# Kernel tuning notes

Hardware: AMD Instinct MI355X
Metric: run time of the kernel (lower is better)

Reference implementation:

```python
import jax, jax.numpy as jnp
import numpy as np

N_NODES = 50000
N_EDGES = 600000
D_IN = 128
D_HID = 128
D_OUT = 40
EPS = 1e-5


def setup_inputs() -> dict:
    key = jax.random.key(0)
    ks = jax.random.split(key, 16)
    inp = {
        "x": jax.random.normal(ks[0], (N_NODES, D_IN), dtype=jnp.float32),
        "edge_index": jax.random.randint(ks[1], (2, N_EDGES), 0, N_NODES, dtype=jnp.int64),
    }
    dims = [(D_IN, D_HID), (D_HID, D_HID), (D_HID, D_OUT)]
    for i, (di, do) in enumerate(dims):
        s = 1.0 / np.sqrt(di)
        inp[f"W_l{i}"] = jax.random.uniform(ks[2 + 3 * i], (di, do), jnp.float32, -s, s)
        inp[f"b_l{i}"] = jax.random.uniform(ks[3 + 3 * i], (do,), jnp.float32, -s, s)
        inp[f"W_r{i}"] = jax.random.uniform(ks[4 + 3 * i], (di, do), jnp.float32, -s, s)
    for i in range(2):  # num_convs - 1 Trans (LayerNorm) blocks
        inp[f"g{i}"] = jnp.ones((D_HID,), jnp.float32)
        inp[f"be{i}"] = jnp.zeros((D_HID,), jnp.float32)
    return inp


def _sage_conv(x, src, dst, W_l, b_l, W_r):
    # mean-aggregate neighbor features at dst, then lin_l(agg) + lin_r(x)
    msg = jax.ops.segment_sum(x[src], dst, num_segments=N_NODES)  # [N, d]
    deg = jax.ops.segment_sum(jnp.ones((src.shape[0],), x.dtype), dst, num_segments=N_NODES)
    agg = msg / jnp.clip(deg, 1.0)[:, None]
    return agg @ W_l + b_l + x @ W_r


def _trans(x, g, b):
    # LayerNorm -> GELU (exact); Dropout p=0 is identity
    mu = jnp.mean(x, axis=-1, keepdims=True)
    var = jnp.mean(jnp.square(x - mu), axis=-1, keepdims=True)
    xn = (x - mu) * jax.lax.rsqrt(var + EPS) * g + b
    return jax.nn.gelu(xn, approximate=False)


def reference(x, edge_index, W_l0, b_l0, W_r0, W_l1, b_l1, W_r1, W_l2, b_l2, W_r2, g0, be0, g1, be1):
    src, dst = edge_index[0], edge_index[1]
    h = _sage_conv(x, src, dst, W_l0, b_l0, W_r0)
    h = _sage_conv(_trans(h, g0, be0), src, dst, W_l1, b_l1, W_r1)
    h = _sage_conv(_trans(h, g1, be1), src, dst, W_l2, b_l2, W_r2)
    return jax.nn.log_softmax(h, axis=1)
```

## Files before the change

### kernel.cpp

```cpp
#include <hip/hip_runtime.h>
#include <math.h>

#define N_NODES 50000
#define N_EDGES 600000
#define DF 128
#define KK 256
#define DOUT 40
#define EPSN 1e-5f
#define NB1 196

typedef __attribute__((ext_vector_type(8))) short sh8;
typedef __attribute__((ext_vector_type(4))) float f32x4;

__device__ __forceinline__ unsigned short f2b(float f) {
  unsigned u = __builtin_bit_cast(unsigned, f);
  unsigned r = u + 0x7FFFu + ((u >> 16) & 1u);
  return (unsigned short)(r >> 16);
}
__device__ __forceinline__ float b2f(unsigned short b) {
  unsigned u = ((unsigned)b) << 16;
  return __builtin_bit_cast(float, u);
}
__device__ __forceinline__ float gelu_f(float x) {
  return 0.5f * x * (1.0f + erff(x * 0.70710678118654752f));
}

__global__ __launch_bounds__(256) void k_prep(
    const int* __restrict__ ei, int* __restrict__ counts,
    const float* __restrict__ x, unsigned* __restrict__ A,
    const float* __restrict__ Wl0, const float* __restrict__ Wr0,
    const float* __restrict__ Wl1, const float* __restrict__ Wr1,
    const float* __restrict__ Wl2, const float* __restrict__ Wr2,
    unsigned short* __restrict__ WT0, unsigned short* __restrict__ WT1,
    unsigned short* __restrict__ WT2b) {
  const int b = blockIdx.x, t = threadIdx.x;
  if (b < 2344) {
    int e = b * 256 + t;
    if (e < N_EDGES) atomicAdd(&counts[ei[N_EDGES + e]], 1);
  } else if (b < 14844) {
    int i = (b - 2344) * 256 + t;
    int n = i >> 6, p = i & 63;
    float2 v = ((const float2*)x)[i];
    A[(size_t)n * 128 + 64 + p] = (unsigned)f2b(v.x) | ((unsigned)f2b(v.y) << 16);
  } else {
    int i = (b - 14844) * 256 + t;
    if (i >= 75776) return;
    if (i < 65536) {
      const float* Wl; const float* Wr; unsigned short* WT; int j;
      if (i < 32768) { j = i;         Wl = Wl0; Wr = Wr0; WT = WT0; }
      else           { j = i - 32768; Wl = Wl1; Wr = Wr1; WT = WT1; }
      int n = j >> 8, k = j & 255;
      float v = (k < DF) ? Wl[k * DF + n] : Wr[(k - DF) * DF + n];
      WT[(k >> 3) * 1024 + n * 8 + (k & 7)] = f2b(v);
    } else {
      int j = i - 65536;
      int n = j >> 7, k = j & 127;
      float v = (n < DOUT) ? Wl2[k * DOUT + n] : Wr2[k * DOUT + (n - DOUT)];
      WT2b[(k >> 3) * 640 + n * 8 + (k & 7)] = f2b(v);
    }
  }
}

__global__ __launch_bounds__(256) void k_rowptr(
    const int* __restrict__ counts,
    int* __restrict__ rowptr, int* __restrict__ cursor,
    float* __restrict__ invdeg) {
  const int t = threadIdx.x;
  const int lane = t & 63, w = t >> 6;
  __shared__ int wtot[4], wpre[4];

  int pre = 0;
  const int limit = blockIdx.x * 256;
  for (int i = t; i < limit; i += 256) pre += counts[i];
  #pragma unroll
  for (int m = 1; m < 64; m <<= 1) pre += __shfl_xor(pre, m);
  if (lane == 0) wpre[w] = pre;

  const int i = blockIdx.x * 256 + t;
  int c = (i < N_NODES) ? counts[i] : 0;
  int s = c;
  #pragma unroll
  for (int off = 1; off < 64; off <<= 1) {
    int u = __shfl_up(s, off);
    if (lane >= off) s += u;
  }
  if (lane == 63) wtot[w] = s;
  __syncthreads();
  int add = wpre[0] + wpre[1] + wpre[2] + wpre[3];
  for (int k = 0; k < w; ++k) add += wtot[k];
  if (i < N_NODES) {
    int excl = s - c + add;
    rowptr[i] = excl;
    cursor[i] = excl;
    invdeg[i] = 1.0f / (float)((c > 1) ? c : 1);
  }
  if (blockIdx.x == 0 && t == 0) rowptr[N_NODES] = N_EDGES;
}

__global__ __launch_bounds__(256) void k_fill(
    const int* __restrict__ ei, int* __restrict__ cursor, int* __restrict__ csr) {
  int e = blockIdx.x * 256 + threadIdx.x;
  if (e < N_EDGES) {
    int d = ei[N_EDGES + e];
    int p = atomicAdd(&cursor[d], 1);
    csr[p] = ei[e];
  }
}

__global__ __launch_bounds__(256) void k_agg(
    unsigned* __restrict__ A, const int* __restrict__ rowptr,
    const int* __restrict__ csr, const float* __restrict__ invdeg) {
  const int wid = (blockIdx.x * 256 + threadIdx.x) >> 6;
  const int lane = threadIdx.x & 63;
  const int sg = lane >> 4, l = lane & 15;
  const int node = wid * 4 + sg;
  const int beg = rowptr[node], end = rowptr[node + 1];
  const uint4* H4 = (const uint4*)A;

  float f0=0,f1=0,f2=0,f3=0,f4=0,f5=0,f6=0,f7=0;
  float g0=0,g1=0,g2=0,g3=0,g4=0,g5=0,g6=0,g7=0;
  int j = beg;
  for (; j + 2 <= end; j += 2) {
    int c0 = csr[j], c1 = csr[j + 1];
    uint4 p = H4[(size_t)c0 * 32 + 16 + l];
    uint4 q = H4[(size_t)c1 * 32 + 16 + l];
    f0 += b2f((unsigned short)p.x); f1 += b2f((unsigned short)(p.x >> 16));
    f2 += b2f((unsigned short)p.y); f3 += b2f((unsigned short)(p.y >> 16));
    f4 += b2f((unsigned short)p.z); f5 += b2f((unsigned short)(p.z >> 16));
    f6 += b2f((unsigned short)p.w); f7 += b2f((unsigned short)(p.w >> 16));
    g0 += b2f((unsigned short)q.x); g1 += b2f((unsigned short)(q.x >> 16));
    g2 += b2f((unsigned short)q.y); g3 += b2f((unsigned short)(q.y >> 16));
    g4 += b2f((unsigned short)q.z); g5 += b2f((unsigned short)(q.z >> 16));
    g6 += b2f((unsigned short)q.w); g7 += b2f((unsigned short)(q.w >> 16));
  }
  if (j < end) {
    uint4 p = H4[(size_t)csr[j] * 32 + 16 + l];
    f0 += b2f((unsigned short)p.x); f1 += b2f((unsigned short)(p.x >> 16));
    f2 += b2f((unsigned short)p.y); f3 += b2f((unsigned short)(p.y >> 16));
    f4 += b2f((unsigned short)p.z); f5 += b2f((unsigned short)(p.z >> 16));
    f6 += b2f((unsigned short)p.w); f7 += b2f((unsigned short)(p.w >> 16));
  }
  f0+=g0; f1+=g1; f2+=g2; f3+=g3; f4+=g4; f5+=g5; f6+=g6; f7+=g7;
  const float rd = invdeg[node];
  uint4 o;
  o.x = (unsigned)f2b(f0 * rd) | ((unsigned)f2b(f1 * rd) << 16);
  o.y = (unsigned)f2b(f2 * rd) | ((unsigned)f2b(f3 * rd) << 16);
  o.z = (unsigned)f2b(f4 * rd) | ((unsigned)f2b(f5 * rd) << 16);
  o.w = (unsigned)f2b(f6 * rd) | ((unsigned)f2b(f7 * rd) << 16);
  ((uint4*)A)[(size_t)node * 32 + l] = o;
}

__global__ __launch_bounds__(256) void k_gemm128(
    const unsigned short* __restrict__ Acat, const unsigned short* __restrict__ WT,
    const float* __restrict__ bl, const float* __restrict__ g,
    const float* __restrict__ be, unsigned short* __restrict__ Adst) {
  __shared__ __align__(16) char lds[8704];
  unsigned short* olds = (unsigned short*)lds;
  float2* pp = (float2*)(lds + 8192);

  const int t = threadIdx.x;
  const int rw = blockIdx.x * 16;
  const int wave = t >> 6, lane = t & 63;
  const int lr = lane & 15, lg = lane >> 4;

  #pragma unroll
  for (int it = 0; it < 2; ++it) {
    int id = it * 256 + t;
    int r = id >> 5, c = id & 31;
    sh8 v = *(const sh8*)(Acat + (size_t)(rw + r) * KK + c * 8);
    unsigned off = (unsigned)((r * 512 + c * 16) ^ ((r & 7) << 4));
    *(sh8*)(lds + off) = v;
  }

  sh8 Bfrag[2][8];
  {
    const sh8* Bp = (const sh8*)WT;
    #pragma unroll
    for (int fl = 0; fl < 2; ++fl) {
      const int n = wave * 32 + fl * 16 + lr;
      #pragma unroll
      for (int ks = 0; ks < 8; ++ks) Bfrag[fl][ks] = Bp[(ks * 4 + lg) * 128 + n];
    }
  }
  const int col0 = wave * 32 + lr, col1 = col0 + 16;
  const float bc0 = bl[col0], bc1 = bl[col1];
  const float gv0 = g[col0], gv1 = g[col1];
  const float bev0 = be[col0], bev1 = be[col1];

  __syncthreads();

  f32x4 acc0 = {0.f, 0.f, 0.f, 0.f}, acc1 = {0.f, 0.f, 0.f, 0.f};
  #pragma unroll
  for (int ks = 0; ks < 8; ++ks) {
    unsigned off = (unsigned)((lr * 512 + ks * 64 + lg * 16) ^ ((lr & 7) << 4));
    sh8 a = *(const sh8*)(lds + off);
    acc0 = __builtin_amdgcn_mfma_f32_16x16x32_bf16(a, Bfrag[0][ks], acc0, 0, 0, 0);
    acc1 = __builtin_amdgcn_mfma_f32_16x16x32_bf16(a, Bfrag[1][ks], acc1, 0, 0, 0);
  }

  float sv[4], qv[4];
  #pragma unroll
  for (int r = 0; r < 4; ++r) {
    float v0 = acc0[r] + bc0, v1 = acc1[r] + bc1;
    acc0[r] = v0; acc1[r] = v1;
    sv[r] = v0 + v1; qv[r] = v0 * v0 + v1 * v1;
  }
  #pragma unroll
  for (int m = 1; m < 16; m <<= 1) {
    #pragma unroll
    for (int r = 0; r < 4; ++r) {
      sv[r] += __shfl_xor(sv[r], m);
      qv[r] += __shfl_xor(qv[r], m);
    }
  }
  if (lr == 0) {
    #pragma unroll
    for (int r = 0; r < 4; ++r)
      pp[wave * 16 + lg * 4 + r] = make_float2(sv[r], qv[r]);
  }
  __syncthreads();

  #pragma unroll
  for (int r = 0; r < 4; ++r) {
    const int row = lg * 4 + r;
    float2 a0 = pp[row], a1 = pp[16 + row], a2 = pp[32 + row], a3 = pp[48 + row];
    float mu = (a0.x + a1.x + a2.x + a3.x) * (1.0f / 128.0f);
    float var = (a0.y + a1.y + a2.y + a3.y) * (1.0f / 128.0f) - mu * mu;
    float rs = rsqrtf(var + EPSN);
    float xn0 = (acc0[r] - mu) * rs * gv0 + bev0;
    float xn1 = (acc1[r] - mu) * rs * gv1 + bev1;
    olds[row * 136 + col0] = f2b(gelu_f(xn0));
    olds[row * 136 + col1] = f2b(gelu_f(xn1));
  }
  __syncthreads();

  {
    int r = t >> 4, c = t & 15;
    sh8 v = *(const sh8*)((char*)olds + r * 272 + c * 16);
    *(sh8*)(Adst + (size_t)(rw + r) * KK + 128 + c * 8) = v;
  }
}

__global__ __launch_bounds__(256) void k_gemm80(
    const unsigned short* __restrict__ Acat, const unsigned short* __restrict__ WT2b,
    unsigned short* __restrict__ PQ) {
  __shared__ __align__(16) char lds[16384];
  const int t = threadIdx.x;
  const int rw = blockIdx.x * 64;
  const int wave = t >> 6, lane = t & 63;
  const int lr = lane & 15, lg = lane >> 4;

  #pragma unroll
  for (int it = 0; it < 4; ++it) {
    int id = it * 256 + t;
    int r = id >> 4, c = id & 15;
    int gr = rw + r; if (gr >= N_NODES) gr = N_NODES - 1;
    sh8 v = *(const sh8*)(Acat + (size_t)gr * KK + 128 + c * 8);
    unsigned off = (unsigned)((r * 256 + c * 16) ^ ((r & 7) << 4));
    *(sh8*)(lds + off) = v;
  }

  sh8 Bfrag[5][4];
  {
    const sh8* Bp = (const sh8*)WT2b;
    #pragma unroll
    for (int f = 0; f < 5; ++f) {
      const int n = f * 16 + lr;
      #pragma unroll
      for (int ks = 0; ks < 4; ++ks) Bfrag[f][ks] = Bp[(ks * 4 + lg) * 80 + n];
    }
  }
  __syncthreads();

  f32x4 accs[5];
  #pragma unroll
  for (int f = 0; f < 5; ++f) accs[f] = (f32x4){0.f, 0.f, 0.f, 0.f};

  #pragma unroll
  for (int ks = 0; ks < 4; ++ks) {
    const int r = wave * 16 + lr;
    unsigned off = (unsigned)((r * 256 + ks * 64 + lg * 16) ^ ((r & 7) << 4));
    sh8 a = *(const sh8*)(lds + off);
    #pragma unroll
    for (int f = 0; f < 5; ++f)
      accs[f] = __builtin_amdgcn_mfma_f32_16x16x32_bf16(a, Bfrag[f][ks], accs[f], 0, 0, 0);
  }
  __syncthreads();

  unsigned short* olds = (unsigned short*)lds;
  #pragma unroll
  for (int f = 0; f < 5; ++f) {
    #pragma unroll
    for (int r = 0; r < 4; ++r) {
      const int row = wave * 16 + lg * 4 + r;
      olds[row * 80 + f * 16 + lr] = f2b(accs[f][r]);
    }
  }
  __syncthreads();

  #pragma unroll
  for (int it = 0; it < 3; ++it) {
    int id = it * 256 + t;
    if (id < 640) {
      int r = (id * 6554) >> 16;
      int c = id - r * 10;
      int gr = rw + r;
      if (gr < N_NODES)
        *(sh8*)(PQ + (size_t)gr * 80 + c * 8) =
            *(const sh8*)((char*)olds + r * 160 + c * 16);
    }
  }
}

__global__ __launch_bounds__(256) void k_final(
    const unsigned short* __restrict__ PQ, const float* __restrict__ bl,
    const int* __restrict__ rowptr, const int* __restrict__ csr,
    const float* __restrict__ invdeg, float* __restrict__ out) {
  const int node = blockIdx.x * 8 + (threadIdx.x >> 5);
  const int hl = threadIdx.x & 31;
  const bool act = (hl < 20);
  const int l = act ? hl : 0;
  const unsigned* Pu = (const unsigned*)PQ;

  const int beg = rowptr[node], end = rowptr[node + 1];
  float ax = 0.f, ay = 0.f, bx = 0.f, by = 0.f;
  float cx = 0.f, cy = 0.f, dx = 0.f, dy = 0.f;
  int j = beg;
  for (; j + 4 <= end; j += 4) {
    int c0 = csr[j], c1 = csr[j + 1], c2 = csr[j + 2], c3 = csr[j + 3];
    unsigned p0 = Pu[(size_t)c0 * 40 + l];
    unsigned p1 = Pu[(size_t)c1 * 40 + l];
    unsigned p2 = Pu[(size_t)c2 * 40 + l];
    unsigned p3 = Pu[(size_t)c3 * 40 + l];
    ax += b2f((unsigned short)p0); ay += b2f((unsigned short)(p0 >> 16));
    bx += b2f((unsigned short)p1); by += b2f((unsigned short)(p1 >> 16));
    cx += b2f((unsigned short)p2); cy += b2f((unsigned short)(p2 >> 16));
    dx += b2f((unsigned short)p3); dy += b2f((unsigned short)(p3 >> 16));
  }
  for (; j < end; ++j) {
    unsigned p = Pu[(size_t)csr[j] * 40 + l];
    ax += b2f((unsigned short)p); ay += b2f((unsigned short)(p >> 16));
  }
  ax += bx + cx + dx;
  ay += by + cy + dy;
  const float rd = invdeg[node];
  unsigned q = Pu[(size_t)node * 40 + 20 + l];
  float v0 = ax * rd + b2f((unsigned short)q) + bl[2 * l];
  float v1 = ay * rd + b2f((unsigned short)(q >> 16)) + bl[2 * l + 1];

  float m = act ? fmaxf(v0, v1) : -INFINITY;
  #pragma unroll
  for (int k = 1; k < 32; k <<= 1) m = fmaxf(m, __shfl_xor(m, k));
  float se = act ? (expf(v0 - m) + expf(v1 - m)) : 0.0f;
  #pragma unroll
  for (int k = 1; k < 32; k <<= 1) se += __shfl_xor(se, k);
  float lse = m + logf(se);
  if (act)
    ((float2*)out)[(size_t)node * 20 + hl] = make_float2(v0 - lse, v1 - lse);
}

extern "C" void kernel_launch(void* const* d_in, const int* in_sizes, int n_in,
                              void* d_out, int out_size, void* d_ws, size_t ws_size,
                              hipStream_t stream) {
  const float* x   = (const float*)d_in[0];
  const int*   ei  = (const int*)d_in[1];
  const float* Wl0 = (const float*)d_in[2];
  const float* bl0 = (const float*)d_in[3];
  const float* Wr0 = (const float*)d_in[4];
  const float* Wl1 = (const float*)d_in[5];
  const float* bl1 = (const float*)d_in[6];
  const float* Wr1 = (const float*)d_in[7];
  const float* Wl2 = (const float*)d_in[8];
  const float* bl2 = (const float*)d_in[9];
  const float* Wr2 = (const float*)d_in[10];
  const float* g0  = (const float*)d_in[11];
  const float* be0 = (const float*)d_in[12];
  const float* g1  = (const float*)d_in[13];
  const float* be1 = (const float*)d_in[14];
  float* out = (float*)d_out;

  unsigned short* A    = (unsigned short*)d_ws;
  unsigned short* PQ   = A + (size_t)N_NODES * KK;
  unsigned short* WT0  = PQ + (size_t)N_NODES * 80;
  unsigned short* WT1  = WT0 + 128 * KK;
  unsigned short* WT2b = WT1 + 128 * KK;
  float* invdeg = (float*)(WT2b + 80 * 128);
  int*   counts = (int*)(invdeg + N_NODES);
  int*   rowptr = counts + N_NODES;
  int*   cursor = rowptr + N_NODES + 1;
  int*   csr    = cursor + N_NODES;

  const int egrid = (N_EDGES + 255) / 256;
  const int pgrid = 2344 + 12500 + 296;
  const int agrid = N_NODES / 16;
  const int g128  = N_NODES / 16;
  const int g80   = (N_NODES + 63) / 64;
  const int fgrid = N_NODES / 8;

  hipMemsetAsync(counts, 0, N_NODES * sizeof(int), stream);
  k_prep<<<pgrid, 256, 0, stream>>>(ei, counts, x, (unsigned*)A,
                                    Wl0, Wr0, Wl1, Wr1, Wl2, Wr2,
                                    WT0, WT1, WT2b);
  k_rowptr<<<NB1, 256, 0, stream>>>(counts, rowptr, cursor, invdeg);
  k_fill<<<egrid, 256, 0, stream>>>(ei, cursor, csr);

  k_agg<<<agrid, 256, 0, stream>>>((unsigned*)A, rowptr, csr, invdeg);
  k_gemm128<<<g128, 256, 0, stream>>>(A, WT0, bl0, g0, be0, A);

  k_agg<<<agrid, 256, 0, stream>>>((unsigned*)A, rowptr, csr, invdeg);
  k_gemm128<<<g128, 256, 0, stream>>>(A, WT1, bl1, g1, be1, A);

  k_gemm80<<<g80, 256, 0, stream>>>(A, WT2b, PQ);
  k_final<<<fgrid, 256, 0, stream>>>(PQ, bl2, rowptr, csr, invdeg, out);
}
```

Baseline: 215.1 us.

## Fuse neighbor aggregation into the SAGE GEMM kernel with ping-pong feature buffers

Merges the separate aggregation kernel into the 128-wide GEMM+LayerNorm+GELU kernel. Each block gathers and averages neighbor rows for its 16 nodes directly into LDS next to its own features, so the aggregated half of the concatenated activation never goes to global memory and is never read back. The interleaved 256-wide A buffer is replaced by two 128-wide buffers used alternately, so the kernel never reads and writes the same buffer. Two fewer launches and less global traffic are gained. The cost is that the irregular gather now runs inside the GEMM block, which may reduce occupancy or let the gather latency stall the MFMA work.

```diff
diff --git a/kernel.cpp b/kernel.cpp
--- a/kernel.cpp
+++ b/kernel.cpp
@@ -27,7 +27,7 @@
 
 __global__ __launch_bounds__(256) void k_prep(
     const int* __restrict__ ei, int* __restrict__ counts,
-    const float* __restrict__ x, unsigned* __restrict__ A,
+    const float* __restrict__ x, unsigned* __restrict__ X0u,
     const float* __restrict__ Wl0, const float* __restrict__ Wr0,
     const float* __restrict__ Wl1, const float* __restrict__ Wr1,
     const float* __restrict__ Wl2, const float* __restrict__ Wr2,
@@ -39,9 +39,8 @@
     if (e < N_EDGES) atomicAdd(&counts[ei[N_EDGES + e]], 1);
   } else if (b < 14844) {
     int i = (b - 2344) * 256 + t;
-    int n = i >> 6, p = i & 63;
     float2 v = ((const float2*)x)[i];
-    A[(size_t)n * 128 + 64 + p] = (unsigned)f2b(v.x) | ((unsigned)f2b(v.y) << 16);
+    X0u[i] = (unsigned)f2b(v.x) | ((unsigned)f2b(v.y) << 16);
   } else {
     int i = (b - 14844) * 256 + t;
     if (i >= 75776) return;
@@ -107,53 +106,12 @@
   }
 }
 
-__global__ __launch_bounds__(256) void k_agg(
-    unsigned* __restrict__ A, const int* __restrict__ rowptr,
-    const int* __restrict__ csr, const float* __restrict__ invdeg) {
-  const int wid = (blockIdx.x * 256 + threadIdx.x) >> 6;
-  const int lane = threadIdx.x & 63;
-  const int sg = lane >> 4, l = lane & 15;
-  const int node = wid * 4 + sg;
-  const int beg = rowptr[node], end = rowptr[node + 1];
-  const uint4* H4 = (const uint4*)A;
-
-  float f0=0,f1=0,f2=0,f3=0,f4=0,f5=0,f6=0,f7=0;
-  float g0=0,g1=0,g2=0,g3=0,g4=0,g5=0,g6=0,g7=0;
-  int j = beg;
-  for (; j + 2 <= end; j += 2) {
-    int c0 = csr[j], c1 = csr[j + 1];
-    uint4 p = H4[(size_t)c0 * 32 + 16 + l];
-    uint4 q = H4[(size_t)c1 * 32 + 16 + l];
-    f0 += b2f((unsigned short)p.x); f1 += b2f((unsigned short)(p.x >> 16));
-    f2 += b2f((unsigned short)p.y); f3 += b2f((unsigned short)(p.y >> 16));
-    f4 += b2f((unsigned short)p.z); f5 += b2f((unsigned short)(p.z >> 16));
-    f6 += b2f((unsigned short)p.w); f7 += b2f((unsigned short)(p.w >> 16));
-    g0 += b2f((unsigned short)q.x); g1 += b2f((unsigned short)(q.x >> 16));
-    g2 += b2f((unsigned short)q.y); g3 += b2f((unsigned short)(q.y >> 16));
-    g4 += b2f((unsigned short)q.z); g5 += b2f((unsigned short)(q.z >> 16));
-    g6 += b2f((unsigned short)q.w); g7 += b2f((unsigned short)(q.w >> 16));
-  }
-  if (j < end) {
-    uint4 p = H4[(size_t)csr[j] * 32 + 16 + l];
-    f0 += b2f((unsigned short)p.x); f1 += b2f((unsigned short)(p.x >> 16));
-    f2 += b2f((unsigned short)p.y); f3 += b2f((unsigned short)(p.y >> 16));
-    f4 += b2f((unsigned short)p.z); f5 += b2f((unsigned short)(p.z >> 16));
-    f6 += b2f((unsigned short)p.w); f7 += b2f((unsigned short)(p.w >> 16));
-  }
-  f0+=g0; f1+=g1; f2+=g2; f3+=g3; f4+=g4; f5+=g5; f6+=g6; f7+=g7;
-  const float rd = invdeg[node];
-  uint4 o;
-  o.x = (unsigned)f2b(f0 * rd) | ((unsigned)f2b(f1 * rd) << 16);
-  o.y = (unsigned)f2b(f2 * rd) | ((unsigned)f2b(f3 * rd) << 16);
-  o.z = (unsigned)f2b(f4 * rd) | ((unsigned)f2b(f5 * rd) << 16);
-  o.w = (unsigned)f2b(f6 * rd) | ((unsigned)f2b(f7 * rd) << 16);
-  ((uint4*)A)[(size_t)node * 32 + l] = o;
-}
-
-__global__ __launch_bounds__(256) void k_gemm128(
-    const unsigned short* __restrict__ Acat, const unsigned short* __restrict__ WT,
+__global__ __launch_bounds__(256) void k_sage128(
+    const unsigned short* __restrict__ Xsrc, const unsigned short* __restrict__ WT,
     const float* __restrict__ bl, const float* __restrict__ g,
-    const float* __restrict__ be, unsigned short* __restrict__ Adst) {
+    const float* __restrict__ be,
+    const int* __restrict__ rowptr, const int* __restrict__ csr,
+    const float* __restrict__ invdeg, unsigned short* __restrict__ Xdst) {
   __shared__ __align__(16) char lds[8704];
   unsigned short* olds = (unsigned short*)lds;
   float2* pp = (float2*)(lds + 8192);
@@ -163,13 +121,51 @@
   const int wave = t >> 6, lane = t & 63;
   const int lr = lane & 15, lg = lane >> 4;
 
-  #pragma unroll
-  for (int it = 0; it < 2; ++it) {
-    int id = it * 256 + t;
-    int r = id >> 5, c = id & 31;
-    sh8 v = *(const sh8*)(Acat + (size_t)(rw + r) * KK + c * 8);
-    unsigned off = (unsigned)((r * 512 + c * 16) ^ ((r & 7) << 4));
+  {
+    int r = t >> 4, c = t & 15;
+    sh8 v = *(const sh8*)(Xsrc + (size_t)(rw + r) * DF + c * 8);
+    unsigned off = (unsigned)((r * 512 + 256 + c * 16) ^ ((r & 7) << 4));
     *(sh8*)(lds + off) = v;
+  }
+
+  {
+    const int sg = lane >> 4, l = lane & 15;
+    const int r = wave * 4 + sg;
+    const int node = rw + r;
+    const int beg = rowptr[node], end = rowptr[node + 1];
+    const uint4* X4 = (const uint4*)Xsrc;
+
+    float f0=0,f1=0,f2=0,f3=0,f4=0,f5=0,f6=0,f7=0;
+    float g0=0,g1=0,g2=0,g3=0,g4=0,g5=0,g6=0,g7=0;
+    int j = beg;
+    for (; j + 2 <= end; j += 2) {
+      int c0 = csr[j], c1 = csr[j + 1];
+      uint4 p = X4[(size_t)c0 * 16 + l];
+      uint4 q = X4[(size_t)c1 * 16 + l];
+      f0 += b2f((unsigned short)p.x); f1 += b2f((unsigned short)(p.x >> 16));
+      f2 += b2f((unsigned short)p.y); f3 += b2f((unsigned short)(p.y >> 16));
+      f4 += b2f((unsigned short)p.z); f5 += b2f((unsigned short)(p.z >> 16));
+      f6 += b2f((unsigned short)p.w); f7 += b2f((unsigned short)(p.w >> 16));
+      g0 += b2f((unsigned short)q.x); g1 += b2f((unsigned short)(q.x >> 16));
+      g2 += b2f((unsigned short)q.y); g3 += b2f((unsigned short)(q.y >> 16));
+      g4 += b2f((unsigned short)q.z); g5 += b2f((unsigned short)(q.z >> 16));
+      g6 += b2f((unsigned short)q.w); g7 += b2f((unsigned short)(q.w >> 16));
+    }
+    if (j < end) {
+      uint4 p = X4[(size_t)csr[j] * 16 + l];
+      f0 += b2f((unsigned short)p.x); f1 += b2f((unsigned short)(p.x >> 16));
+      f2 += b2f((unsigned short)p.y); f3 += b2f((unsigned short)(p.y >> 16));
+      f4 += b2f((unsigned short)p.z); f5 += b2f((unsigned short)(p.z >> 16));
+      f6 += b2f((unsigned short)p.w); f7 += b2f((unsigned short)(p.w >> 16));
+    }
+    f0+=g0; f1+=g1; f2+=g2; f3+=g3; f4+=g4; f5+=g5; f6+=g6; f7+=g7;
+    const float rd = invdeg[node];
+    uint4 o;
+    o.x = (unsigned)f2b(f0 * rd) | ((unsigned)f2b(f1 * rd) << 16);
+    o.y = (unsigned)f2b(f2 * rd) | ((unsigned)f2b(f3 * rd) << 16);
+    o.z = (unsigned)f2b(f4 * rd) | ((unsigned)f2b(f5 * rd) << 16);
+    o.w = (unsigned)f2b(f6 * rd) | ((unsigned)f2b(f7 * rd) << 16);
+    *(uint4*)(lds + ((unsigned)(r * 512 + l * 16) ^ ((r & 7) << 4))) = o;
   }
 
   sh8 Bfrag[2][8];
@@ -237,12 +233,12 @@
   {
     int r = t >> 4, c = t & 15;
     sh8 v = *(const sh8*)((char*)olds + r * 272 + c * 16);
-    *(sh8*)(Adst + (size_t)(rw + r) * KK + 128 + c * 8) = v;
+    *(sh8*)(Xdst + (size_t)(rw + r) * DF + c * 8) = v;
   }
 }
 
 __global__ __launch_bounds__(256) void k_gemm80(
-    const unsigned short* __restrict__ Acat, const unsigned short* __restrict__ WT2b,
+    const unsigned short* __restrict__ X, const unsigned short* __restrict__ WT2b,
     unsigned short* __restrict__ PQ) {
   __shared__ __align__(16) char lds[16384];
   const int t = threadIdx.x;
@@ -255,7 +251,7 @@
     int id = it * 256 + t;
     int r = id >> 4, c = id & 15;
     int gr = rw + r; if (gr >= N_NODES) gr = N_NODES - 1;
-    sh8 v = *(const sh8*)(Acat + (size_t)gr * KK + 128 + c * 8);
+    sh8 v = *(const sh8*)(X + (size_t)gr * DF + c * 8);
     unsigned off = (unsigned)((r * 256 + c * 16) ^ ((r & 7) << 4));
     *(sh8*)(lds + off) = v;
   }
@@ -379,8 +375,9 @@
   const float* be1 = (const float*)d_in[14];
   float* out = (float*)d_out;
 
-  unsigned short* A    = (unsigned short*)d_ws;
-  unsigned short* PQ   = A + (size_t)N_NODES * KK;
+  unsigned short* X0   = (unsigned short*)d_ws;
+  unsigned short* X1   = X0 + (size_t)N_NODES * DF;
+  unsigned short* PQ   = X1 + (size_t)N_NODES * DF;
   unsigned short* WT0  = PQ + (size_t)N_NODES * 80;
   unsigned short* WT1  = WT0 + 128 * KK;
   unsigned short* WT2b = WT1 + 128 * KK;
@@ -392,24 +389,20 @@
 
   const int egrid = (N_EDGES + 255) / 256;
   const int pgrid = 2344 + 12500 + 296;
-  const int agrid = N_NODES / 16;
-  const int g128  = N_NODES / 16;
+  const int sgrid = N_NODES / 16;
   const int g80   = (N_NODES + 63) / 64;
   const int fgrid = N_NODES / 8;
 
   hipMemsetAsync(counts, 0, N_NODES * sizeof(int), stream);
-  k_prep<<<pgrid, 256, 0, stream>>>(ei, counts, x, (unsigned*)A,
+  k_prep<<<pgrid, 256, 0, stream>>>(ei, counts, x, (unsigned*)X0,
                                     Wl0, Wr0, Wl1, Wr1, Wl2, Wr2,
                                     WT0, WT1, WT2b);
   k_rowptr<<<NB1, 256, 0, stream>>>(counts, rowptr, cursor, invdeg);
   k_fill<<<egrid, 256, 0, stream>>>(ei, cursor, csr);
 
-  k_agg<<<agrid, 256, 0, stream>>>((unsigned*)A, rowptr, csr, invdeg);
-  k_gemm128<<<g128, 256, 0, stream>>>(A, WT0, bl0, g0, be0, A);
-
-  k_agg<<<agrid, 256, 0, stream>>>((unsigned*)A, rowptr, csr, invdeg);
-  k_gemm128<<<g128, 256, 0, stream>>>(A, WT1, bl1, g1, be1, A);
-
-  k_gemm80<<<g80, 256, 0, stream>>>(A, WT2b, PQ);
+  k_sage128<<<sgrid, 256, 0, stream>>>(X0, WT0, bl0, g0, be0, rowptr, csr, invdeg, X1);
+  k_sage128<<<sgrid, 256, 0, stream>>>(X1, WT1, bl1, g1, be1, rowptr, csr, invdeg, X0);
+
+  k_gemm80<<<g80, 256, 0, stream>>>(X0, WT2b, PQ);
   k_final<<<fgrid, 256, 0, stream>>>(PQ, bl2, rowptr, csr, invdeg, out);
 }
```

Result: slower. 219.5 us (+2.1%).
